# Kernel optimization log

Measured on AMD Instinct MI355X. Metric: run time of the kernel, lower is better.

## Reference

```python
import jax, jax.numpy as jnp
import numpy as np

LSTM = 256
NUM_CELLS = 5
BLOCKS = 6
TEMP = 5.0
TANH_C = 1.1


def setup_inputs() -> dict:
    key = jax.random.key(0)
    ks = jax.random.split(key, 8)
    s = 0.05  # small init so sigmoids/tanh stay in sane range
    return {
        "enc_w": jax.random.normal(ks[0], (5, LSTM), jnp.float32) * s,
        "w_ih": jax.random.normal(ks[1], (4 * LSTM, LSTM), jnp.float32) * s,
        "w_hh": jax.random.normal(ks[2], (4 * LSTM, LSTM), jnp.float32) * s,
        "b_ih": jax.random.normal(ks[3], (4 * LSTM,), jnp.float32) * s,
        "b_hh": jax.random.normal(ks[4], (4 * LSTM,), jnp.float32) * s,
        "w1": jax.random.normal(ks[5], (LSTM, LSTM), jnp.float32) * s,
        "w2": jax.random.normal(ks[6], (LSTM, LSTM), jnp.float32) * s,
        "v": jax.random.normal(ks[7], (LSTM,), jnp.float32) * s,
    }


def _lstm_cell(x, h, c, w_ih, w_hh, b_ih, b_hh):
    # torch.nn.LSTMCell gate order: i, f, g, o
    g = w_ih @ x + b_ih + w_hh @ h + b_hh  # [4*LSTM]
    i, f, gg, o = jnp.split(g, 4)
    i, f, o = jax.nn.sigmoid(i), jax.nn.sigmoid(f), jax.nn.sigmoid(o)
    c2 = f * c + i * jnp.tanh(gg)
    h2 = o * jnp.tanh(c2)
    return h2, c2


def _run_sampler(bkey, enc_w, w_ih, w_hh, b_ih, b_hh, w1, w2, v):
    zeros = jnp.zeros((LSTM,), jnp.float32)
    inputs = enc_w[0]  # encoder(0)
    anchors = []
    anchors_w1 = []
    prev_h = prev_c = zeros
    # first two layers: LSTM always fed zero state (faithful to source)
    for _ in range(2):
        prev_h, prev_c = _lstm_cell(inputs, zeros, zeros, w_ih, w_hh, b_ih, b_hh)
        anchors.append(zeros)
        anchors_w1.append(w1 @ prev_h)
    arc_seq, log_probs, entropies = [], [], []
    step = 0
    for layer_id in range(2, NUM_CELLS + 2):
        for _ in range(2):
            prev_h, prev_c = _lstm_cell(inputs, prev_h, prev_c, w_ih, w_hh, b_ih, b_hh)
            q = jnp.tanh(jnp.stack(anchors_w1[:layer_id]) + w2 @ prev_h)  # [layer_id, LSTM]
            logits = (q @ v) / TEMP  # [layer_id]
            logits = TANH_C * jnp.tanh(logits)
            skey = jax.random.fold_in(bkey, step); step += 1
            index = jax.random.categorical(skey, logits)
            lsm = jax.nn.log_softmax(logits)
            arc_seq.append(index)
            log_probs.append(-lsm[index])  # F.cross_entropy
            entropies.append(jax.lax.stop_gradient(-jnp.sum(lsm * jnp.exp(lsm))))
            inputs = jnp.stack(anchors[:layer_id])[index]
        prev_h, prev_c = _lstm_cell(inputs, prev_h, prev_c, w_ih, w_hh, b_ih, b_hh)
        anchors.append(prev_h)
        anchors_w1.append(w1 @ prev_h)
        inputs = enc_w[0]
    arc = jnp.stack(arc_seq)  # [2*NUM_CELLS] int
    return arc, sum(entropies), sum(log_probs), prev_c, prev_h


def reference(enc_w, w_ih, w_hh, b_ih, b_hh, w1, w2, v):
    key = jax.random.key(42)
    all_arc = []
    all_entropy = jnp.float32(0.0)
    all_log_prob = jnp.float32(0.0)
    c = h = None
    for b in range(BLOCKS):
        arc, ent, lp, c, h = _run_sampler(
            jax.random.fold_in(key, b), enc_w, w_ih, w_hh, b_ih, b_hh, w1, w2, v)
        all_arc.append(arc)
        all_entropy = all_entropy + ent
        all_log_prob = all_log_prob + lp
    return (jnp.stack(all_arc), all_log_prob, all_entropy, c[None, :], h[None, :])
```

## Files before the change

kernel.cpp:

```cpp
#include <hip/hip_runtime.h>
#include <stdint.h>


#define NBLK  6
#define PWG   8
#define TINYF 1.17549435e-38f
#define XTAG  0xC3B00000u
#define DONE_MAGIC 0x444f4e45

typedef unsigned long long u64;
struct U2 { uint32_t x, y; };

#define V10_DONE 0u
#define V10_PART 64u
#define V10_EX   512u
#define V10_NEED 221696u

#define S_READY 0u
#define S_DONE  192u
#define S_PART  224u
#define S_HP    320u
#define S_ACC   24896u
#define FXS     67108864.0f
#define READY_MAGIC 0x52454459

__device__ __forceinline__ U2 tf2x32(uint32_t k0, uint32_t k1,
                                     uint32_t c0, uint32_t c1) {
  uint32_t ks2 = k0 ^ k1 ^ 0x1BD11BDAu;
  uint32_t x0 = c0 + k0, x1 = c1 + k1;
#define TFR(r) { x0 += x1; x1 = (x1 << (r)) | (x1 >> (32 - (r))); x1 ^= x0; }
  TFR(13) TFR(15) TFR(26) TFR(6)   x0 += k1;  x1 += ks2 + 1u;
  TFR(17) TFR(29) TFR(16) TFR(24)  x0 += ks2; x1 += k0 + 2u;
  TFR(13) TFR(15) TFR(26) TFR(6)   x0 += k0;  x1 += k1 + 3u;
  TFR(17) TFR(29) TFR(16) TFR(24)  x0 += k1;  x1 += ks2 + 4u;
  TFR(13) TFR(15) TFR(26) TFR(6)   x0 += ks2; x1 += k0 + 5u;
#undef TFR
  U2 r; r.x = x0; r.y = x1; return r;
}

__device__ __forceinline__ float sigf(float x) {
  return 1.0f / (1.0f + expf(-x));
}
__device__ __forceinline__ void istore(int* p, int v) {
  __hip_atomic_store(p, v, __ATOMIC_RELAXED, __HIP_MEMORY_SCOPE_AGENT);
}
__device__ __forceinline__ int iload(const int* p) {
  return __hip_atomic_load(p, __ATOMIC_RELAXED, __HIP_MEMORY_SCOPE_AGENT);
}
__device__ __forceinline__ void hstore(u64* p, u64 v) {
  __hip_atomic_store(p, v, __ATOMIC_RELAXED, __HIP_MEMORY_SCOPE_AGENT);
}
__device__ __forceinline__ u64 hload(const u64* p) {
  return __hip_atomic_load(p, __ATOMIC_RELAXED, __HIP_MEMORY_SCOPE_AGENT);
}
__device__ __forceinline__ void fstore(float* p, float v) {
  __hip_atomic_store(p, v, __ATOMIC_RELAXED, __HIP_MEMORY_SCOPE_AGENT);
}
__device__ __forceinline__ float fload(const float* p) {
  return __hip_atomic_load(p, __ATOMIC_RELAXED, __HIP_MEMORY_SCOPE_AGENT);
}

__global__ __launch_bounds__(1024) void ctrl_v10(
    const float* __restrict__ enc_w,
    const float* __restrict__ wih,
    const float* __restrict__ whh,
    const float* __restrict__ b_ih,
    const float* __restrict__ b_hh,
    const float* __restrict__ w1,
    const float* __restrict__ w2,
    const float* __restrict__ vvec,
    unsigned char* __restrict__ ws,
    float* __restrict__ out) {

  const int b = blockIdx.x & 7;
  const int p = blockIdx.x >> 3;
  if (b >= NBLK) return;
  const int tid = threadIdx.x;

  int*   done = (int*)(ws + V10_DONE);
  float* part = (float*)(ws + V10_PART);
  u64*   ex   = (u64*)(ws + V10_EX);

  const int rl = tid & 127, s = tid >> 7;
  const int g = rl >> 5, el = rl & 31;
  const int row = g * 256 + p * 32 + el;
  const int k0 = s * 32;
  const int rr = tid & 255, ks = tid >> 8;

  __shared__ __align__(16) float gateL[1024];
  __shared__ __align__(16) float hL[256], encL[256], vL[256];
  __shared__ __align__(16) float anchL[4][256];
  __shared__ __align__(16) float w2hS[256], aw1S[6][256];
  __shared__ float rowSumL[128], biasS[128], h2S[32];
  __shared__ float logitL[8];
  __shared__ int   selL;

  if (tid < 256) { encL[tid] = enc_w[tid]; vL[tid] = vvec[tid]; }
  if (tid < 128) {
    int r = (tid >> 5) * 256 + p * 32 + (tid & 31);
    biasS[tid] = b_ih[r] + b_hh[r];
  }

  float4 wihr[8], whhr[8];
  #pragma unroll
  for (int c = 0; c < 8; ++c) {
    int cc = (c + s) & 7;
    wihr[c] = *(const float4*)(wih + row * 256 + k0 + cc * 4);
    whhr[c] = *(const float4*)(whh + row * 256 + k0 + cc * 4);
  }
  float w1c[8], w2c[8];
  #pragma unroll
  for (int j = 0; j < 8; ++j) {
    w1c[j] = w1[rr * 256 + p * 32 + ks * 8 + j];
    w2c[j] = w2[rr * 256 + p * 32 + ks * 8 + j];
  }
  __syncthreads();

  auto dotIH = [&](const float* x) {
    float a = 0.0f;
    #pragma unroll
    for (int c = 0; c < 8; ++c) {
      int cc = (c + s) & 7;
      float4 xv = *(const float4*)(x + k0 + cc * 4);
      float4 w = wihr[c];
      a += w.x * xv.x + w.y * xv.y + w.z * xv.z + w.w * xv.w;
    }
    return a;
  };
  auto dotHH = [&]() {
    float a = 0.0f;
    #pragma unroll
    for (int c = 0; c < 8; ++c) {
      int cc = (c + s) & 7;
      float4 xv = *(const float4*)(hL + k0 + cc * 4);
      float4 w = whhr[c];
      a += w.x * xv.x + w.y * xv.y + w.z * xv.z + w.w * xv.w;
    }
    return a;
  };

  const float encih = dotIH(encL);

  float cv = 0.0f;
  U2 bk = tf2x32(0u, 42u, 0u, (uint32_t)b);
  int k = 1, step = 0;
  float lpAcc = 0.0f, entAcc = 0.0f;

  auto cell = [&](float gacc, int mode, int aid, int cid) {
    gateL[tid] = gacc;
    __syncthreads();
    if (tid < 128) {
      float ssum = 0.0f;
      #pragma unroll
      for (int j = 0; j < 8; ++j) ssum += gateL[j * 128 + tid];
      rowSumL[tid] = ssum + biasS[tid];
    }
    __syncthreads();
    if (tid < 32) {
      float gi = rowSumL[tid],       gf = rowSumL[32 + tid];
      float gg2 = rowSumL[64 + tid], go = rowSumL[96 + tid];
      float c2 = sigf(gf) * cv + sigf(gi) * tanhf(gg2);
      float h2 = sigf(go) * tanhf(c2);
      cv = c2;
      h2S[tid] = h2;
      if (mode == 2 && b == NBLK - 1) {
        out[62 + p * 32 + tid] = cv;
        out[318 + p * 32 + tid] = h2;
      }
    }
    __syncthreads();
    if (mode == 2) return;

    {
      const float* wc = (mode == 1) ? w1c : w2c;
      float yp = 0.0f;
      #pragma unroll
      for (int j = 0; j < 8; ++j) yp += wc[j] * h2S[ks * 8 + j];
      gateL[tid] = yp;
    }
    __syncthreads();
    const uint32_t tagk = XTAG | (uint32_t)k;
    u64* slot = ex + (((size_t)(k & 1) * NBLK + b) * PWG + p) * 288;
    if (tid < 256) {
      float yo = (gateL[tid] + gateL[256 + tid]) +
                 (gateL[512 + tid] + gateL[768 + tid]);
      hstore(slot + tid, ((u64)tagk << 32) | (u64)__float_as_uint(yo));
    } else if (tid < 288) {
      hstore(slot + tid,
             ((u64)tagk << 32) | (u64)__float_as_uint(h2S[tid - 256]));
    }
    __syncthreads();
    {
      int e = tid & 255, q = tid >> 8;
      const u64* base = ex + (((size_t)(k & 1) * NBLK + b) * PWG) * 288;
      const u64* pa = base + (2 * q) * 288 + e;
      const u64* pb = base + (2 * q + 1) * 288 + e;
      const u64* ph = base + (tid >> 5) * 288 + 256 + (tid & 31);
      u64 va = 0, vb = 0, vh = 0;
      bool da = false, db = false, dh = (tid >= 256);
      for (;;) {
        if (!da) { va = hload(pa); da = ((uint32_t)(va >> 32) == tagk); }
        if (!db) { vb = hload(pb); db = ((uint32_t)(vb >> 32) == tagk); }
        if (!dh) { vh = hload(ph); dh = ((uint32_t)(vh >> 32) == tagk); }
        if (da && db && dh) break;
        __builtin_amdgcn_s_sleep(1);
      }
      gateL[tid] = __uint_as_float((uint32_t)va) +
                   __uint_as_float((uint32_t)vb);
      float hv = __uint_as_float((uint32_t)vh);
      __syncthreads();
      if (tid < 256) {
        float y = (gateL[tid] + gateL[256 + tid]) +
                  (gateL[512 + tid] + gateL[768 + tid]);
        if (mode == 1) aw1S[aid][tid] = y; else w2hS[tid] = y;
        hL[tid] = hv;
        if (mode == 1 && cid >= 0) anchL[cid][tid] = hv;
      }
    }
    __syncthreads();
    ++k;
  };

  auto sample = [&](int L) -> int {
    int wv = tid >> 6, lane = tid & 63;
    if (wv < L) {
      float a = 0.0f;
      #pragma unroll
      for (int j = 0; j < 4; ++j) {
        int kk = j * 64 + lane;
        a += tanhf(aw1S[wv][kk] + w2hS[kk]) * vL[kk];
      }
      a += __shfl_down(a, 32);
      a += __shfl_down(a, 16);
      a += __shfl_down(a, 8);
      a += __shfl_down(a, 4);
      a += __shfl_down(a, 2);
      a += __shfl_down(a, 1);
      if (lane == 0) logitL[wv] = a;
    }
    __syncthreads();
    if (tid < 64) {
      float lg = 0.0f, sgum = -1e30f;
      if (tid < L) {
        lg = 1.1f * tanhf(logitL[tid] * 0.2f);
        U2 sk = tf2x32(bk.x, bk.y, 0u, (uint32_t)step);
        U2 r2 = tf2x32(sk.x, sk.y, 0u, (uint32_t)tid);
        uint32_t bits = r2.x ^ r2.y;
        float u = __uint_as_float((bits >> 9) | 0x3f800000u) - 1.0f;
        u = fmaxf(TINYF, u + TINYF);
        sgum = lg - logf(-logf(u));
      }
      int bi = 0;
      float best = __shfl(sgum, 0, 64);
      for (int j = 1; j < L; ++j) {
        float sj = __shfl(sgum, j, 64);
        if (sj > best) { best = sj; bi = j; }
      }
      float mx = __shfl(lg, 0, 64);
      for (int j = 1; j < L; ++j) mx = fmaxf(mx, __shfl(lg, j, 64));
      float se = 0.0f;
      for (int j = 0; j < L; ++j) se += expf(__shfl(lg, j, 64) - mx);
      float lse = logf(se);
      float lgbi = __shfl(lg, bi, 64);
      float es = 0.0f;
      for (int j = 0; j < L; ++j) {
        float l = __shfl(lg, j, 64) - mx - lse;
        es += l * expf(l);
      }
      if (tid == 0) {
        lpAcc += -(lgbi - mx - lse);
        entAcc += -es;
        selL = bi;
        if (p == 0) out[b * 10 + step] = (float)bi;
      }
    }
    __syncthreads();
    step++;
    return selL;
  };

  cell(encih, 1, 0, -1);
  if (tid < 256) aw1S[1][tid] = aw1S[0][tid];
  __syncthreads();

  for (int L = 2; L <= 6; ++L) {
    cell(encih + dotHH(), 0, 0, -1);
    int s1v = sample(L);
    {
      float a = (s1v >= 2) ? dotIH(&anchL[s1v - 2][0]) : 0.0f;
      cell(a + dotHH(), 0, 0, -1);
    }
    int s2v = sample(L);
    {
      float a = (s2v >= 2) ? dotIH(&anchL[s2v - 2][0]) : 0.0f;
      if (L < 6) cell(a + dotHH(), 1, L, L - 2);
      else       cell(a + dotHH(), 2, 0, -1);
    }
  }

  if (p == 0 && tid == 0) {
    fstore(&part[2 * b], lpAcc);
    fstore(&part[2 * b + 1], entAcc);
    __builtin_amdgcn_s_waitcnt(0);
    istore(&done[b], DONE_MAGIC);
    if (b == NBLK - 1) {
      float lp = 0.0f, en = 0.0f;
      for (int j = 0; j < NBLK; ++j) {
        while (iload(&done[j]) != DONE_MAGIC) __builtin_amdgcn_s_sleep(1);
        lp += fload(&part[2 * j]);
        en += fload(&part[2 * j + 1]);
      }
      out[60] = lp;
      out[61] = en;
    }
  }
}

__global__ __launch_bounds__(1024) void ctrl_small(
    const float* __restrict__ enc_w,
    const float* __restrict__ wih,
    const float* __restrict__ whh,
    const float* __restrict__ b_ih,
    const float* __restrict__ b_hh,
    const float* __restrict__ w1,
    const float* __restrict__ w2,
    const float* __restrict__ vvec,
    unsigned char* __restrict__ ws,
    float* __restrict__ out) {

  const int b = blockIdx.x & 7;
  const int p = blockIdx.x >> 3;
  if (b >= NBLK) return;
  const int tid = threadIdx.x;

  int*   ready = (int*)(ws + S_READY);
  int*   done  = (int*)(ws + S_DONE);
  float* part  = (float*)(ws + S_PART);
  u64*   hp    = (u64*)(ws + S_HP);
  int*   acc   = (int*)(ws + S_ACC);

  const int rl = tid >> 3, s = tid & 7;
  const int g = rl >> 5, el = rl & 31;
  const int row = g * 256 + p * 32 + el;
  const int k0 = s * 32;
  const int rr = tid & 255, ks = tid >> 8;

  __shared__ __align__(16) float hL[256], encL[256], vL[256];
  __shared__ __align__(16) float anchL[4][256];
  __shared__ __align__(16) float partL[1024];
  __shared__ __align__(16) float w2hS[256], aw1S[6][256];
  __shared__ float rowSumL[128], biasS[128], h2S[32];
  __shared__ float logitL[8];
  __shared__ int   selL;

  if (tid < 256) { encL[tid] = enc_w[tid]; vL[tid] = vvec[tid]; }
  if (tid < 128) {
    int gg = tid >> 5, ee = tid & 31, r = gg * 256 + p * 32 + ee;
    biasS[tid] = b_ih[r] + b_hh[r];
  }

  float4 wihr[8], whhr[8];
  #pragma unroll
  for (int c = 0; c < 8; ++c) {
    int cc = (c + s) & 7;
    wihr[c] = *(const float4*)(wih + row * 256 + k0 + cc * 4);
    whhr[c] = *(const float4*)(whh + row * 256 + k0 + cc * 4);
  }
  float w1c[8], w2c[8];
  #pragma unroll
  for (int j = 0; j < 8; ++j) {
    w1c[j] = w1[rr * 256 + p * 32 + ks * 8 + j];
    w2c[j] = w2[rr * 256 + p * 32 + ks * 8 + j];
  }

  if (tid < 32) istore(&acc[1 * (NBLK * 256) + b * 256 + p * 32 + tid], 0);
  __syncthreads();
  if (tid == 0) istore(&ready[b * 8 + p], READY_MAGIC);
  if (tid < 8) {
    while (iload(&ready[b * 8 + tid]) != READY_MAGIC)
      __builtin_amdgcn_s_sleep(1);
  }
  __syncthreads();

  auto dotIH = [&](const float* x) {
    float a = 0.0f;
    #pragma unroll
    for (int c = 0; c < 8; ++c) {
      int cc = (c + s) & 7;
      float4 xv = *(const float4*)(x + k0 + cc * 4);
      float4 w = wihr[c];
      a += w.x * xv.x + w.y * xv.y + w.z * xv.z + w.w * xv.w;
    }
    return a;
  };
  auto dotHH = [&]() {
    float a = 0.0f;
    #pragma unroll
    for (int c = 0; c < 8; ++c) {
      int cc = (c + s) & 7;
      float4 xv = *(const float4*)(hL + k0 + cc * 4);
      float4 w = whhr[c];
      a += w.x * xv.x + w.y * xv.y + w.z * xv.z + w.w * xv.w;
    }
    return a;
  };

  const float encih = dotIH(encL);
  float cv = 0.0f;
  U2 bk = tf2x32(0u, 42u, 0u, (uint32_t)b);
  int k = 1, step = 0;
  float lpAcc = 0.0f, entAcc = 0.0f;

  auto cell = [&](float gacc, int mode, int aid, int cid) {
    partL[tid] = gacc;
    __syncthreads();
    if (tid < 128) {
      float ssum = 0.0f;
      #pragma unroll
      for (int j = 0; j < 8; ++j) ssum += partL[tid * 8 + j];
      rowSumL[tid] = ssum + biasS[tid];
    }
    __syncthreads();
    if (tid < 32) {
      float gi = rowSumL[tid],       gf = rowSumL[32 + tid];
      float gg2 = rowSumL[64 + tid], go = rowSumL[96 + tid];
      float c2 = sigf(gf) * cv + sigf(gi) * tanhf(gg2);
      float h2 = sigf(go) * tanhf(c2);
      cv = c2;
      h2S[tid] = h2;
      if (mode == 2 && b == NBLK - 1) {
        out[62 + p * 32 + tid] = cv;
        out[318 + p * 32 + tid] = h2;
      }
    }
    __syncthreads();
    if (mode == 2) return;
    {
      const float* wc = (mode == 1) ? w1c : w2c;
      float yp = 0.0f;
      #pragma unroll
      for (int j = 0; j < 8; ++j) yp += wc[j] * h2S[ks * 8 + j];
      atomicAdd(&acc[(k % 3) * (NBLK * 256) + b * 256 + rr],
                __float2int_rn(yp * FXS));
      if (tid < 32)
        istore(&acc[((k + 1) % 3) * (NBLK * 256) + b * 256 + p * 32 + tid], 0);
    }
    __syncthreads();
    if (tid < 32) {
      u64 pk = ((u64)(uint32_t)k << 32) | (u64)__float_as_uint(h2S[tid]);
      hstore(&hp[(k & 1) * (NBLK * 256) + b * 256 + p * 32 + tid], pk);
    }
    if (tid < 256) {
      u64 v;
      const u64* src = &hp[(k & 1) * (NBLK * 256) + b * 256 + tid];
      while ((int)(hload(src) >> 32) != k) __builtin_amdgcn_s_sleep(1);
      v = hload(src);
      float hv = __uint_as_float((uint32_t)v);
      hL[tid] = hv;
      if (mode == 1 && cid >= 0) anchL[cid][tid] = hv;
    }
    __syncthreads();
    if (tid < 256) {
      int iv = iload(&acc[(k % 3) * (NBLK * 256) + b * 256 + tid]);
      float f = (float)((double)iv * (1.0 / 67108864.0));
      if (mode == 1) aw1S[aid][tid] = f; else w2hS[tid] = f;
    }
    __syncthreads();
    ++k;
  };

  auto sample = [&](int L) -> int {
    int wv = tid >> 6, lane = tid & 63;
    if (wv < L) {
      float a = 0.0f;
      #pragma unroll
      for (int j = 0; j < 4; ++j) {
        int kk = lane * 4 + j;
        a += tanhf(aw1S[wv][kk] + w2hS[kk]) * vL[kk];
      }
      a += __shfl_down(a, 32);
      a += __shfl_down(a, 16);
      a += __shfl_down(a, 8);
      a += __shfl_down(a, 4);
      a += __shfl_down(a, 2);
      a += __shfl_down(a, 1);
      if (lane == 0) logitL[wv] = a;
    }
    __syncthreads();
    if (tid < 64) {
      float lg = 0.0f, sgum = -1e30f;
      if (tid < L) {
        lg = 1.1f * tanhf(logitL[tid] * 0.2f);
        U2 sk = tf2x32(bk.x, bk.y, 0u, (uint32_t)step);
        U2 r2 = tf2x32(sk.x, sk.y, 0u, (uint32_t)tid);
        uint32_t bits = r2.x ^ r2.y;
        float u = __uint_as_float((bits >> 9) | 0x3f800000u) - 1.0f;
        u = fmaxf(TINYF, u + TINYF);
        sgum = lg - logf(-logf(u));
      }
      int bi = 0;
      float best = __shfl(sgum, 0, 64);
      for (int j = 1; j < L; ++j) {
        float sj = __shfl(sgum, j, 64);
        if (sj > best) { best = sj; bi = j; }
      }
      float mx = __shfl(lg, 0, 64);
      for (int j = 1; j < L; ++j) mx = fmaxf(mx, __shfl(lg, j, 64));
      float se = 0.0f;
      for (int j = 0; j < L; ++j) se += expf(__shfl(lg, j, 64) - mx);
      float lse = logf(se);
      float lgbi = __shfl(lg, bi, 64);
      float es = 0.0f;
      for (int j = 0; j < L; ++j) {
        float l = __shfl(lg, j, 64) - mx - lse;
        es += l * expf(l);
      }
      if (tid == 0) {
        lpAcc += -(lgbi - mx - lse);
        entAcc += -es;
        selL = bi;
        if (p == 0) out[b * 10 + step] = (float)bi;
      }
    }
    __syncthreads();
    step++;
    return selL;
  };

  cell(encih, 1, 0, -1);
  if (tid < 256) aw1S[1][tid] = aw1S[0][tid];
  __syncthreads();
  for (int L = 2; L <= 6; ++L) {
    cell(encih + dotHH(), 0, 0, -1);
    int s1v = sample(L);
    {
      float a = (s1v >= 2) ? dotIH(&anchL[s1v - 2][0]) : 0.0f;
      cell(a + dotHH(), 0, 0, -1);
    }
    int s2v = sample(L);
    {
      float a = (s2v >= 2) ? dotIH(&anchL[s2v - 2][0]) : 0.0f;
      if (L < 6) cell(a + dotHH(), 1, L, L - 2);
      else       cell(a + dotHH(), 2, 0, -1);
    }
  }
  if (p == 0 && tid == 0) {
    fstore(&part[2 * b], lpAcc);
    fstore(&part[2 * b + 1], entAcc);
    __builtin_amdgcn_s_waitcnt(0);
    istore(&done[b], DONE_MAGIC);
    if (b == NBLK - 1) {
      float lp = 0.0f, en = 0.0f;
      for (int j = 0; j < NBLK; ++j) {
        while (iload(&done[j]) != DONE_MAGIC) __builtin_amdgcn_s_sleep(1);
        lp += fload(&part[2 * j]);
        en += fload(&part[2 * j + 1]);
      }
      out[60] = lp;
      out[61] = en;
    }
  }
}

extern "C" void kernel_launch(void* const* d_in, const int* in_sizes, int n_in,
                              void* d_out, int out_size, void* d_ws, size_t ws_size,
                              hipStream_t stream) {
  const float* enc = (const float*)d_in[0];
  const float* wih = (const float*)d_in[1];
  const float* whh = (const float*)d_in[2];
  const float* bih = (const float*)d_in[3];
  const float* bhh = (const float*)d_in[4];
  const float* w1  = (const float*)d_in[5];
  const float* w2  = (const float*)d_in[6];
  const float* v   = (const float*)d_in[7];
  unsigned char* ws = (unsigned char*)d_ws;
  float* out = (float*)d_out;

  if (ws_size >= V10_NEED) {
    ctrl_v10<<<dim3(64), dim3(1024), 0, stream>>>(
        enc, wih, whh, bih, bhh, w1, w2, v, ws, out);
  } else {
    ctrl_small<<<dim3(64), dim3(1024), 0, stream>>>(
        enc, wih, whh, bih, bhh, w1, w2, v, ws, out);
  }
}
```

Baseline: 158.3 us.

## Centralize sampling in one workgroup and split h/y exchange across workgroups

Workgroups drop from 1024 to 512 threads, with each thread holding twice as many weight columns in registers. The cross-workgroup exchange is split in two: h slices go to a per-block buffer that every workgroup polls, while w1/w2 projection partials are packed two floats per word behind one tag. Only workgroup p==0 gathers the projections and runs sampling, then publishes the chosen index that the other workgroups poll for. This is meant to cut exchange traffic and redundant sampling work, and to overlap the next dotHH with waiting for the index. In exchange it adds a serial dependency on p==0 and raises register pressure per thread.

```diff
diff --git a/kernel.cpp b/kernel.cpp
--- a/kernel.cpp
+++ b/kernel.cpp
@@ -4,17 +4,22 @@
 
 #define NBLK  6
 #define PWG   8
+#define THR   512
 #define TINYF 1.17549435e-38f
-#define XTAG  0xC3B00000u
+#define HTAGB 0xC3B00000u
+#define YTAGB 0xE1700000u
+#define ITAGB 0xA5D00000u
 #define DONE_MAGIC 0x444f4e45
 
 typedef unsigned long long u64;
 struct U2 { uint32_t x, y; };
 
-#define V10_DONE 0u
-#define V10_PART 64u
-#define V10_EX   512u
-#define V10_NEED 221696u
+#define W_DONE 0u
+#define W_PART 64u
+#define W_IDX  128u
+#define W_HX   640u
+#define W_YMB  25216u
+#define W_NEED 126976u
 
 #define S_READY 0u
 #define S_DONE  192u
@@ -59,8 +64,16 @@
 __device__ __forceinline__ float fload(const float* p) {
   return __hip_atomic_load(p, __ATOMIC_RELAXED, __HIP_MEMORY_SCOPE_AGENT);
 }
-
-__global__ __launch_bounds__(1024) void ctrl_v10(
+__device__ __forceinline__ u64 pollw(const u64* p, uint32_t want) {
+  u64 v;
+  for (;;) {
+    v = hload(p);
+    if ((uint32_t)(v >> 32) == want) return v;
+    __builtin_amdgcn_s_sleep(1);
+  }
+}
+
+__global__ __launch_bounds__(THR, 2) void ctrl_v11(
     const float* __restrict__ enc_w,
     const float* __restrict__ wih,
     const float* __restrict__ whh,
@@ -77,20 +90,23 @@
   if (b >= NBLK) return;
   const int tid = threadIdx.x;
 
-  int*   done = (int*)(ws + V10_DONE);
-  float* part = (float*)(ws + V10_PART);
-  u64*   ex   = (u64*)(ws + V10_EX);
+  int*   done = (int*)(ws + W_DONE);
+  float* part = (float*)(ws + W_PART);
+  u64*   idxw = (u64*)(ws + W_IDX);
+  u64*   hx   = (u64*)(ws + W_HX);
+  u64*   ymb  = (u64*)(ws + W_YMB);
 
   const int rl = tid & 127, s = tid >> 7;
-  const int g = rl >> 5, el = rl & 31;
-  const int row = g * 256 + p * 32 + el;
-  const int k0 = s * 32;
+  const int grow = (rl >> 5) * 256 + p * 32 + (rl & 31);
+  const int k0 = s * 64;
   const int rr = tid & 255, ks = tid >> 8;
-
-  __shared__ __align__(16) float gateL[1024];
+  const int cb = p * 32 + ks * 16;
+
+  __shared__ __align__(16) float gateL[THR];
   __shared__ __align__(16) float hL[256], encL[256], vL[256];
   __shared__ __align__(16) float anchL[4][256];
   __shared__ __align__(16) float w2hS[256], aw1S[6][256];
+  __shared__ __align__(16) float yL8[8][256];
   __shared__ float rowSumL[128], biasS[128], h2S[32];
   __shared__ float logitL[8];
   __shared__ int   selL;
@@ -101,27 +117,25 @@
     biasS[tid] = b_ih[r] + b_hh[r];
   }
 
-  float4 wihr[8], whhr[8];
+  float4 wihr[16], whhr[16];
   #pragma unroll
-  for (int c = 0; c < 8; ++c) {
-    int cc = (c + s) & 7;
-    wihr[c] = *(const float4*)(wih + row * 256 + k0 + cc * 4);
-    whhr[c] = *(const float4*)(whh + row * 256 + k0 + cc * 4);
-  }
-  float w1c[8], w2c[8];
+  for (int c = 0; c < 16; ++c) {
+    wihr[c] = *(const float4*)(wih + grow * 256 + k0 + c * 4);
+    whhr[c] = *(const float4*)(whh + grow * 256 + k0 + c * 4);
+  }
+  float w1c[16], w2c[16];
   #pragma unroll
-  for (int j = 0; j < 8; ++j) {
-    w1c[j] = w1[rr * 256 + p * 32 + ks * 8 + j];
-    w2c[j] = w2[rr * 256 + p * 32 + ks * 8 + j];
+  for (int j = 0; j < 16; ++j) {
+    w1c[j] = w1[rr * 256 + cb + j];
+    w2c[j] = w2[rr * 256 + cb + j];
   }
   __syncthreads();
 
   auto dotIH = [&](const float* x) {
     float a = 0.0f;
     #pragma unroll
-    for (int c = 0; c < 8; ++c) {
-      int cc = (c + s) & 7;
-      float4 xv = *(const float4*)(x + k0 + cc * 4);
+    for (int c = 0; c < 16; ++c) {
+      float4 xv = *(const float4*)(x + k0 + c * 4);
       float4 w = wihr[c];
       a += w.x * xv.x + w.y * xv.y + w.z * xv.z + w.w * xv.w;
     }
@@ -130,9 +144,8 @@
   auto dotHH = [&]() {
     float a = 0.0f;
     #pragma unroll
-    for (int c = 0; c < 8; ++c) {
-      int cc = (c + s) & 7;
-      float4 xv = *(const float4*)(hL + k0 + cc * 4);
+    for (int c = 0; c < 16; ++c) {
+      float4 xv = *(const float4*)(hL + k0 + c * 4);
       float4 w = whhr[c];
       a += w.x * xv.x + w.y * xv.y + w.z * xv.z + w.w * xv.w;
     }
@@ -152,7 +165,7 @@
     if (tid < 128) {
       float ssum = 0.0f;
       #pragma unroll
-      for (int j = 0; j < 8; ++j) ssum += gateL[j * 128 + tid];
+      for (int j = 0; j < 4; ++j) ssum += gateL[j * 128 + tid];
       rowSumL[tid] = ssum + biasS[tid];
     }
     __syncthreads();
@@ -163,9 +176,11 @@
       float h2 = sigf(go) * tanhf(c2);
       cv = c2;
       h2S[tid] = h2;
-      if (mode == 2 && b == NBLK - 1) {
-        out[62 + p * 32 + tid] = cv;
-        out[318 + p * 32 + tid] = h2;
+      if (mode == 2) {
+        if (b == NBLK - 1) { out[62 + p * 32 + tid] = cv; out[318 + p * 32 + tid] = h2; }
+      } else {
+        hstore(&hx[(k & 1) * 1536 + b * 256 + p * 32 + tid],
+               ((u64)(HTAGB | (uint32_t)k) << 32) | (u64)__float_as_uint(h2));
       }
     }
     __syncthreads();
@@ -175,126 +190,145 @@
       const float* wc = (mode == 1) ? w1c : w2c;
       float yp = 0.0f;
       #pragma unroll
-      for (int j = 0; j < 8; ++j) yp += wc[j] * h2S[ks * 8 + j];
+      for (int j = 0; j < 16; ++j) yp += wc[j] * h2S[ks * 16 + j];
       gateL[tid] = yp;
     }
     __syncthreads();
-    const uint32_t tagk = XTAG | (uint32_t)k;
-    u64* slot = ex + (((size_t)(k & 1) * NBLK + b) * PWG + p) * 288;
+    u64* mslot = ymb + (size_t)(k & 1) * 6192 + (b * 8 + p) * 129;
+    if (tid < 128) {
+      float ya = gateL[2 * tid]     + gateL[256 + 2 * tid];
+      float yb = gateL[2 * tid + 1] + gateL[256 + 2 * tid + 1];
+      hstore(mslot + tid,
+             ((u64)__float_as_uint(yb) << 32) | (u64)__float_as_uint(ya));
+    }
+    __syncthreads();
+    if (tid == 0)
+      hstore(mslot + 128, ((u64)(YTAGB | (uint32_t)k) << 32) | 1u);
+
     if (tid < 256) {
-      float yo = (gateL[tid] + gateL[256 + tid]) +
-                 (gateL[512 + tid] + gateL[768 + tid]);
-      hstore(slot + tid, ((u64)tagk << 32) | (u64)__float_as_uint(yo));
-    } else if (tid < 288) {
-      hstore(slot + tid,
-             ((u64)tagk << 32) | (u64)__float_as_uint(h2S[tid - 256]));
-    }
-    __syncthreads();
-    {
-      int e = tid & 255, q = tid >> 8;
-      const u64* base = ex + (((size_t)(k & 1) * NBLK + b) * PWG) * 288;
-      const u64* pa = base + (2 * q) * 288 + e;
-      const u64* pb = base + (2 * q + 1) * 288 + e;
-      const u64* ph = base + (tid >> 5) * 288 + 256 + (tid & 31);
-      u64 va = 0, vb = 0, vh = 0;
-      bool da = false, db = false, dh = (tid >= 256);
-      for (;;) {
-        if (!da) { va = hload(pa); da = ((uint32_t)(va >> 32) == tagk); }
-        if (!db) { vb = hload(pb); db = ((uint32_t)(vb >> 32) == tagk); }
-        if (!dh) { vh = hload(ph); dh = ((uint32_t)(vh >> 32) == tagk); }
-        if (da && db && dh) break;
-        __builtin_amdgcn_s_sleep(1);
-      }
-      gateL[tid] = __uint_as_float((uint32_t)va) +
-                   __uint_as_float((uint32_t)vb);
-      float hv = __uint_as_float((uint32_t)vh);
+      u64 v = pollw(&hx[(k & 1) * 1536 + b * 256 + tid], HTAGB | (uint32_t)k);
+      float hv = __uint_as_float((uint32_t)v);
+      hL[tid] = hv;
+      if (mode == 1 && cid >= 0) anchL[cid][tid] = hv;
+    }
+    __syncthreads();
+
+    if (p == 0) {
+      if (tid < 8)
+        pollw(ymb + (size_t)(k & 1) * 6192 + (b * 8 + tid) * 129 + 128,
+              YTAGB | (uint32_t)k);
+      __syncthreads();
+      {
+        int pw = tid >> 6, o = tid & 63;
+        const u64* mb = ymb + (size_t)(k & 1) * 6192 + (b * 8 + pw) * 129;
+        u64 wa = hload(mb + 2 * o), wb = hload(mb + 2 * o + 1);
+        yL8[pw][4 * o + 0] = __uint_as_float((uint32_t)wa);
+        yL8[pw][4 * o + 1] = __uint_as_float((uint32_t)(wa >> 32));
+        yL8[pw][4 * o + 2] = __uint_as_float((uint32_t)wb);
+        yL8[pw][4 * o + 3] = __uint_as_float((uint32_t)(wb >> 32));
+      }
       __syncthreads();
       if (tid < 256) {
-        float y = (gateL[tid] + gateL[256 + tid]) +
-                  (gateL[512 + tid] + gateL[768 + tid]);
+        float y = 0.0f;
+        #pragma unroll
+        for (int pw = 0; pw < 8; ++pw) y += yL8[pw][tid];
         if (mode == 1) aw1S[aid][tid] = y; else w2hS[tid] = y;
-        hL[tid] = hv;
-        if (mode == 1 && cid >= 0) anchL[cid][tid] = hv;
-      }
-    }
-    __syncthreads();
+      }
+      __syncthreads();
+    }
     ++k;
   };
 
-  auto sample = [&](int L) -> int {
-    int wv = tid >> 6, lane = tid & 63;
-    if (wv < L) {
-      float a = 0.0f;
-      #pragma unroll
-      for (int j = 0; j < 4; ++j) {
-        int kk = j * 64 + lane;
-        a += tanhf(aw1S[wv][kk] + w2hS[kk]) * vL[kk];
-      }
-      a += __shfl_down(a, 32);
-      a += __shfl_down(a, 16);
-      a += __shfl_down(a, 8);
-      a += __shfl_down(a, 4);
-      a += __shfl_down(a, 2);
-      a += __shfl_down(a, 1);
-      if (lane == 0) logitL[wv] = a;
-    }
-    __syncthreads();
-    if (tid < 64) {
-      float lg = 0.0f, sgum = -1e30f;
-      if (tid < L) {
-        lg = 1.1f * tanhf(logitL[tid] * 0.2f);
-        U2 sk = tf2x32(bk.x, bk.y, 0u, (uint32_t)step);
-        U2 r2 = tf2x32(sk.x, sk.y, 0u, (uint32_t)tid);
-        uint32_t bits = r2.x ^ r2.y;
-        float u = __uint_as_float((bits >> 9) | 0x3f800000u) - 1.0f;
-        u = fmaxf(TINYF, u + TINYF);
-        sgum = lg - logf(-logf(u));
-      }
-      int bi = 0;
-      float best = __shfl(sgum, 0, 64);
-      for (int j = 1; j < L; ++j) {
-        float sj = __shfl(sgum, j, 64);
-        if (sj > best) { best = sj; bi = j; }
-      }
-      float mx = __shfl(lg, 0, 64);
-      for (int j = 1; j < L; ++j) mx = fmaxf(mx, __shfl(lg, j, 64));
-      float se = 0.0f;
-      for (int j = 0; j < L; ++j) se += expf(__shfl(lg, j, 64) - mx);
-      float lse = logf(se);
-      float lgbi = __shfl(lg, bi, 64);
-      float es = 0.0f;
-      for (int j = 0; j < L; ++j) {
-        float l = __shfl(lg, j, 64) - mx - lse;
-        es += l * expf(l);
-      }
+  auto resolve = [&](int L) -> int {
+    if (p == 0) {
+      int wv = tid >> 6, lane = tid & 63;
+      if (wv < L) {
+        float a = 0.0f;
+        #pragma unroll
+        for (int j = 0; j < 4; ++j) {
+          int kk = j * 64 + lane;
+          a += tanhf(aw1S[wv][kk] + w2hS[kk]) * vL[kk];
+        }
+        a += __shfl_down(a, 32);
+        a += __shfl_down(a, 16);
+        a += __shfl_down(a, 8);
+        a += __shfl_down(a, 4);
+        a += __shfl_down(a, 2);
+        a += __shfl_down(a, 1);
+        if (lane == 0) logitL[wv] = a;
+      }
+      __syncthreads();
+      if (tid < 64) {
+        float lg = 0.0f, sgum = -1e30f;
+        if (tid < L) {
+          lg = 1.1f * tanhf(logitL[tid] * 0.2f);
+          U2 sk = tf2x32(bk.x, bk.y, 0u, (uint32_t)step);
+          U2 r2 = tf2x32(sk.x, sk.y, 0u, (uint32_t)tid);
+          uint32_t bits = r2.x ^ r2.y;
+          float u = __uint_as_float((bits >> 9) | 0x3f800000u) - 1.0f;
+          u = fmaxf(TINYF, u + TINYF);
+          sgum = lg - logf(-logf(u));
+        }
+        int bi = 0;
+        float best = __shfl(sgum, 0, 64);
+        for (int j = 1; j < L; ++j) {
+          float sj = __shfl(sgum, j, 64);
+          if (sj > best) { best = sj; bi = j; }
+        }
+        float mx = __shfl(lg, 0, 64);
+        for (int j = 1; j < L; ++j) mx = fmaxf(mx, __shfl(lg, j, 64));
+        float se = 0.0f;
+        for (int j = 0; j < L; ++j) se += expf(__shfl(lg, j, 64) - mx);
+        float lse = logf(se);
+        float lgbi = __shfl(lg, bi, 64);
+        float es = 0.0f;
+        for (int j = 0; j < L; ++j) {
+          float l = __shfl(lg, j, 64) - mx - lse;
+          es += l * expf(l);
+        }
+        if (tid == 0) {
+          lpAcc += -(lgbi - mx - lse);
+          entAcc += -es;
+          selL = bi;
+          out[b * 10 + step] = (float)bi;
+          hstore(&idxw[b * 10 + step],
+                 ((u64)(ITAGB | (uint32_t)step) << 32) | (u64)(uint32_t)bi);
+        }
+      }
+      __syncthreads();
+    } else {
       if (tid == 0) {
-        lpAcc += -(lgbi - mx - lse);
-        entAcc += -es;
-        selL = bi;
-        if (p == 0) out[b * 10 + step] = (float)bi;
-      }
-    }
-    __syncthreads();
+        u64 v = pollw(&idxw[b * 10 + step], ITAGB | (uint32_t)step);
+        selL = (int)(uint32_t)v;
+      }
+      __syncthreads();
+    }
     step++;
     return selL;
   };
 
   cell(encih, 1, 0, -1);
-  if (tid < 256) aw1S[1][tid] = aw1S[0][tid];
-  __syncthreads();
+  if (p == 0) {
+    if (tid < 256) aw1S[1][tid] = aw1S[0][tid];
+    __syncthreads();
+  }
 
   for (int L = 2; L <= 6; ++L) {
-    cell(encih + dotHH(), 0, 0, -1);
-    int s1v = sample(L);
+    { float hh = dotHH(); cell(encih + hh, 0, 0, -1); }
     {
-      float a = (s1v >= 2) ? dotIH(&anchL[s1v - 2][0]) : 0.0f;
-      cell(a + dotHH(), 0, 0, -1);
-    }
-    int s2v = sample(L);
+      int s1; float hh;
+      if (p == 0) { s1 = resolve(L); hh = dotHH(); }
+      else        { hh = dotHH(); s1 = resolve(L); }
+      float a = (s1 >= 2) ? dotIH(&anchL[s1 - 2][0]) : 0.0f;
+      cell(a + hh, 0, 0, -1);
+    }
     {
-      float a = (s2v >= 2) ? dotIH(&anchL[s2v - 2][0]) : 0.0f;
-      if (L < 6) cell(a + dotHH(), 1, L, L - 2);
-      else       cell(a + dotHH(), 2, 0, -1);
+      int s2; float hh;
+      if (p == 0) { s2 = resolve(L); hh = dotHH(); }
+      else        { hh = dotHH(); s2 = resolve(L); }
+      float a = (s2 >= 2) ? dotIH(&anchL[s2 - 2][0]) : 0.0f;
+      if (L < 6) cell(a + hh, 1, L, L - 2);
+      else       cell(a + hh, 2, 0, -1);
     }
   }
 
@@ -576,8 +610,8 @@
   unsigned char* ws = (unsigned char*)d_ws;
   float* out = (float*)d_out;
 
-  if (ws_size >= V10_NEED) {
-    ctrl_v10<<<dim3(64), dim3(1024), 0, stream>>>(
+  if (ws_size >= W_NEED) {
+    ctrl_v11<<<dim3(64), dim3(THR), 0, stream>>>(
         enc, wih, whh, bih, bhh, w1, w2, v, ws, out);
   } else {
     ctrl_small<<<dim3(64), dim3(1024), 0, stream>>>(
```

After: 152.4 us. 1.04x faster.
